# Optimization experiments

Measured on AMD Instinct MI355X. Metric: run time of the kernel, lower is better.

Reference implementation:

```python
import jax, jax.numpy as jnp
import numpy as np

N = 50000   # nodes
E = 800000  # edges
F = 64      # node_feature_dim
H = 128     # hidden_dim


def setup_inputs() -> dict:
    key = jax.random.key(0)
    ks = jax.random.split(key, 20)
    def w(k, shape, fan_in):
        return jax.random.normal(k, shape, jnp.float32) / np.sqrt(fan_in)
    return {
        "x": jax.random.normal(ks[0], (N, F), jnp.float32),
        "edge_index": jax.random.randint(ks[1], (2, E), 0, N, jnp.int32),
        "enc_w1": w(ks[2], (F, H), F), "enc_b1": jnp.zeros((H,), jnp.float32),
        "enc_w2": w(ks[3], (H, H), H), "enc_b2": jnp.zeros((H,), jnp.float32),
        "w_c1": w(ks[4], (H, H), H), "b_c1": jnp.zeros((H,), jnp.float32),
        "w_c2": w(ks[5], (H, H), H), "b_c2": jnp.zeros((H,), jnp.float32),
        "w_c3": w(ks[6], (H, H), H), "b_c3": jnp.zeros((H,), jnp.float32),
        "dec_w1": w(ks[7], (H, H), H), "dec_b1": jnp.zeros((H,), jnp.float32),
        "dec_w2": w(ks[8], (H, F), H), "dec_b2": jnp.zeros((F,), jnp.float32),
    }


def _gcn_conv(h, W, b, src, dst, dinv):
    # PyG GCNConv: D^-1/2 (A+I) D^-1/2 (h W) + b  (self-loops already in src/dst)
    hw = h @ W                                   # [N, H]
    norm = dinv[src] * dinv[dst]                 # [E+N]
    msg = hw[src] * norm[:, None]                # gather + scale
    return jax.ops.segment_sum(msg, dst, num_segments=N) + b


def reference(x, edge_index, enc_w1, enc_b1, enc_w2, enc_b2,
              w_c1, b_c1, w_c2, b_c2, w_c3, b_c3,
              dec_w1, dec_b1, dec_w2, dec_b2):
    loop = jnp.arange(N, dtype=edge_index.dtype)
    src = jnp.concatenate([edge_index[0], loop])
    dst = jnp.concatenate([edge_index[1], loop])
    deg = jax.ops.segment_sum(jnp.ones_like(dst, jnp.float32), dst, num_segments=N)
    dinv = jax.lax.rsqrt(deg)  # deg >= 1 because of self-loops

    h = jax.nn.relu(x @ enc_w1 + enc_b1) @ enc_w2 + enc_b2  # encoder MLP
    h = jax.nn.relu(_gcn_conv(h, w_c1, b_c1, src, dst, dinv))
    h = jax.nn.relu(_gcn_conv(h, w_c2, b_c2, src, dst, dinv))
    h = jax.nn.relu(_gcn_conv(h, w_c3, b_c3, src, dst, dinv))
    # window_size == 1: chunk+cat is identity
    out = jax.nn.relu(h @ dec_w1 + dec_b1) @ dec_w2 + dec_b2  # decoder MLP
    return jax.nn.sigmoid(out)
```

## Files before the change

### kernel.cpp

```cpp
#include <hip/hip_runtime.h>
#include <stdint.h>

#define NN 50000
#define NE 800000
#define FD 64
#define HD 128
#define NBKT 196
#define BCAP 5120
#define P1E 8192

static_assert(NN % 16 == 0, "aggm16 grid is exact");

typedef __attribute__((ext_vector_type(8))) short short8;
typedef __attribute__((ext_vector_type(4))) float f32x4;

#define AS1 __attribute__((address_space(1)))
#define AS3 __attribute__((address_space(3)))

__device__ __forceinline__ float bflo(unsigned int v) {
    union { unsigned int u; float f; } c; c.u = v << 16; return c.f;
}
__device__ __forceinline__ float bfhi(unsigned int v) {
    union { unsigned int u; float f; } c; c.u = v & 0xffff0000u; return c.f;
}
__device__ __forceinline__ unsigned short f2bf(float f) {
    union { float f; unsigned int u; } c; c.f = f;
    unsigned int u = c.u;
    return (unsigned short)((u + 0x7fffu + ((u >> 16) & 1u)) >> 16);
}
__device__ __forceinline__ unsigned int pack2(float a, float b) {
    return (unsigned int)f2bf(a) | ((unsigned int)f2bf(b) << 16);
}

__global__ void wt0_k(const float* __restrict__ w0, unsigned short* __restrict__ t0) {
    int e = blockIdx.x * 256 + threadIdx.x;
    int k = e >> 7, c = e & 127;
    int gsw = (k >> 3) ^ (c & 7);
    t0[c * 64 + gsw * 8 + (k & 7)] = f2bf(w0[e]);
}

template <int K, int COLS, int EPI, bool BIAS, bool RSCALE, bool A_F32, bool OUT_F32>
__device__ __forceinline__ void mgemm_dev(
    int bid,
    const void* __restrict__ Av,
    const unsigned short* __restrict__ Wt,
    const float* __restrict__ bias,
    const float* __restrict__ dinv,
    void* __restrict__ outv, int nrows)
{
    constexpr int NB = COLS / 16;
    constexpr int KC = K / 32;
    constexpr int GMASK = (K >> 3) - 1;
    __shared__ __align__(16) unsigned char Ws8[COLS * K * 2];

    const int tid = threadIdx.x;
    const int wave = tid >> 6;
    const int lane = tid & 63;

    {
        constexpr int ROUNDS = COLS * K * 2 / 4096;
        const int gb = wave * 1024 + lane * 16;
        const int lb = wave * 1024;
        #pragma unroll
        for (int r = 0; r < ROUNDS; r++) {
            __builtin_amdgcn_global_load_lds(
                (const AS1 unsigned int*)((const unsigned char*)Wt + r * 4096 + gb),
                (AS3 unsigned int*)(Ws8 + r * 4096 + lb),
                16, 0, 0);
        }
    }

    const int m = lane & 15;
    const int q = lane >> 4;
    const int row0 = bid * 64 + wave * 16;

    f32x4 acc[NB];
    #pragma unroll
    for (int i = 0; i < NB; i++) acc[i] = (f32x4){0.f, 0.f, 0.f, 0.f};

    const bool arow_ok = !A_F32 || (row0 + m) < nrows;

    short8 af[KC];
    #pragma unroll
    for (int kc = 0; kc < KC; kc++) {
        if constexpr (A_F32) {
            const float* arowf = (const float*)Av + (size_t)(row0 + m) * K + q * 8 + kc * 32;
            float4 lo = make_float4(0.f, 0.f, 0.f, 0.f), hi = lo;
            if (arow_ok) { lo = *(const float4*)arowf; hi = *(const float4*)(arowf + 4); }
            af[kc][0] = (short)f2bf(lo.x); af[kc][1] = (short)f2bf(lo.y);
            af[kc][2] = (short)f2bf(lo.z); af[kc][3] = (short)f2bf(lo.w);
            af[kc][4] = (short)f2bf(hi.x); af[kc][5] = (short)f2bf(hi.y);
            af[kc][6] = (short)f2bf(hi.z); af[kc][7] = (short)f2bf(hi.w);
        } else {
            const unsigned short* arow = (const unsigned short*)Av + (size_t)(row0 + m) * K + q * 8 + kc * 32;
            af[kc] = *(const short8*)arow;
        }
    }
    __syncthreads();

    #pragma unroll
    for (int kc = 0; kc < KC; kc++) {
        #pragma unroll
        for (int nb = 0; nb < NB; nb++) {
            const int c = nb * 16 + m;
            const int gsw = (kc * 4 + q) ^ (c & GMASK);
            short8 bf = *(const short8*)&Ws8[(c * K + gsw * 8) * 2];
            acc[nb] = __builtin_amdgcn_mfma_f32_16x16x32_bf16(af[kc], bf, acc[nb], 0, 0, 0);
        }
    }

    float bv[NB];
    #pragma unroll
    for (int nb = 0; nb < NB; nb++) bv[nb] = BIAS ? bias[nb * 16 + m] : 0.f;

    #pragma unroll
    for (int r = 0; r < 4; r++) {
        int row = row0 + q * 4 + r;
        if (row < nrows) {
            float sc = RSCALE ? dinv[row] : 1.f;
            #pragma unroll
            for (int nb = 0; nb < NB; nb++) {
                float t = acc[nb][r];
                if (RSCALE) t *= sc;
                t += bv[nb];
                if (EPI == 1) t = fmaxf(t, 0.f);
                if (EPI == 2) t = 1.f / (1.f + __expf(-t));
                if constexpr (OUT_F32) {
                    ((float*)outv)[(size_t)row * COLS + nb * 16 + m] = t;
                } else {
                    ((unsigned short*)outv)[(size_t)row * COLS + nb * 16 + m] = f2bf(t);
                }
            }
        }
    }
}

template <int K, int COLS, int EPI, bool BIAS, bool RSCALE, bool A_F32, bool OUT_F32>
__global__ __launch_bounds__(256) void mgemm_k(
    const void* __restrict__ Av, const unsigned short* __restrict__ Wt,
    const float* __restrict__ bias, const float* __restrict__ dinv,
    void* __restrict__ outv, int nrows)
{
    mgemm_dev<K, COLS, EPI, BIAS, RSCALE, A_F32, OUT_F32>(blockIdx.x, Av, Wt, bias, dinv, outv, nrows);
}

__global__ __launch_bounds__(256) void k1_k(
    const float* __restrict__ x, const unsigned short* __restrict__ t0s,
    const float* __restrict__ enc_b1, unsigned short* __restrict__ bufA,
    const int* __restrict__ src, const int* __restrict__ dst,
    int* __restrict__ gcnt, unsigned int* __restrict__ bucket,
    const float* __restrict__ w1, const float* __restrict__ w2,
    const float* __restrict__ w3, const float* __restrict__ w4,
    const float* __restrict__ w5, const float* __restrict__ w6,
    unsigned short* __restrict__ t1, unsigned short* __restrict__ t2,
    unsigned short* __restrict__ t3, unsigned short* __restrict__ t4,
    unsigned short* __restrict__ t5, unsigned short* __restrict__ t6,
    int gb, int pb)
{
    const int b = blockIdx.x;
    if (b < gb) {
        mgemm_dev<64, 128, 1, true, false, true, false>(b, x, t0s, enc_b1, nullptr, bufA, NN);
    } else if (b < gb + pb) {
        __shared__ int lcnt[256], lsw[256], lexc[256], lofs[256], lrank[256];
        __shared__ unsigned int stage[P1E];
        const int tid = threadIdx.x;
        const int bb = b - gb;
        lcnt[tid] = 0; lrank[tid] = 0;
        __syncthreads();
        unsigned int ent[P1E / 256];
        #pragma unroll
        for (int u = 0; u < P1E / 256; u++) {
            int g = bb * P1E + u * 256 + tid;
            if (g < NE) {
                int d = dst[g], s = src[g];
                int bk = d >> 8;
                atomicAdd(&lcnt[bk], 1);
                ent[u] = (unsigned int)s | ((unsigned int)(d & 255) << 16)
                       | ((unsigned int)bk << 24);
            } else ent[u] = 0xFFFFFFFFu;
        }
        __syncthreads();
        int v = lcnt[tid];
        lsw[tid] = v; __syncthreads();
        for (int d = 1; d < 256; d <<= 1) {
            int xx = (tid >= d) ? lsw[tid - d] : 0; __syncthreads();
            lsw[tid] += xx; __syncthreads();
        }
        lexc[tid] = lsw[tid] - v;
        lofs[tid] = (v > 0) ? atomicAdd(&gcnt[tid], v) : 0;
        __syncthreads();
        #pragma unroll
        for (int u = 0; u < P1E / 256; u++) {
            if (ent[u] != 0xFFFFFFFFu) {
                int bk = ent[u] >> 24;
                int r = atomicAdd(&lrank[bk], 1);
                stage[lexc[bk] + r] = ent[u];
            }
        }
        __syncthreads();
        int cb = NE - bb * P1E; if (cb > P1E) cb = P1E;
        for (int i = tid; i < cb; i += 256) {
            unsigned int e = stage[i];
            int bk = e >> 24;
            bucket[(size_t)bk * BCAP + lofs[bk] + (i - lexc[bk])] = e;
        }
    } else {
        int b2 = b - gb - pb;
        const float* W; unsigned short* T; int C = 128;
        if      (b2 <  64) { W = w1; T = t1; }
        else if (b2 < 128) { W = w2; T = t2; b2 -= 64; }
        else if (b2 < 192) { W = w3; T = t3; b2 -= 128; }
        else if (b2 < 256) { W = w4; T = t4; b2 -= 192; }
        else if (b2 < 320) { W = w5; T = t5; b2 -= 256; }
        else               { W = w6; T = t6; b2 -= 320; C = 64; }
        int e = b2 * 256 + threadIdx.x;
        int k, c;
        if (C == 128) { k = e >> 7; c = e & 127; } else { k = e >> 6; c = e & 63; }
        int gsw = (k >> 3) ^ (c & 15);
        T[c * 128 + gsw * 8 + (k & 7)] = f2bf(W[e]);
    }
}

__global__ __launch_bounds__(256) void k2_k(
    const unsigned short* __restrict__ bufA, const unsigned short* __restrict__ t1,
    const float* __restrict__ enc_b2, unsigned short* __restrict__ bufB,
    const int* __restrict__ gcnt, const unsigned int* __restrict__ bucket,
    int* __restrict__ off, float* __restrict__ dinv,
    unsigned short* __restrict__ csr, int gb)
{
    if ((int)blockIdx.x < gb) {
        mgemm_dev<128, 128, 0, true, false, false, false>(blockIdx.x, bufA, t1, enc_b2, nullptr, bufB, NN);
    } else {
        __shared__ int lc[256], sw[256], sexc[256], lr[256], gsh[256];
        const int tid = threadIdx.x;
        const int b = blockIdx.x - gb;
        int gv = (tid < NBKT) ? gcnt[tid] : 0;
        gsh[tid] = gv; __syncthreads();
        for (int d = 1; d < 256; d <<= 1) {
            int xx = (tid >= d) ? gsh[tid - d] : 0; __syncthreads();
            gsh[tid] += xx; __syncthreads();
        }
        const int cb = gcnt[b];
        const int base = gsh[b] - cb;
        unsigned int ent[BCAP / 256];
        #pragma unroll
        for (int u = 0; u < BCAP / 256; u++) {
            int i = u * 256 + tid;
            ent[u] = (i < cb) ? bucket[(size_t)b * BCAP + i] : 0xFFFFFFFFu;
        }
        lc[tid] = 0; lr[tid] = 0;
        __syncthreads();
        #pragma unroll
        for (int u = 0; u < BCAP / 256; u++)
            if (ent[u] != 0xFFFFFFFFu) atomicAdd(&lc[(ent[u] >> 16) & 255], 1);
        __syncthreads();
        int v = lc[tid];
        int node = b * 256 + tid;
        if (node < NN) dinv[node] = rsqrtf((float)(v + 1));
        sw[tid] = v; __syncthreads();
        for (int d = 1; d < 256; d <<= 1) {
            int xx = (tid >= d) ? sw[tid - d] : 0; __syncthreads();
            sw[tid] += xx; __syncthreads();
        }
        sexc[tid] = sw[tid] - v;
        if (node < NN) off[node] = base + sexc[tid];
        if (b == NBKT - 1 && tid == 0) off[NN] = NE;
        __syncthreads();
        #pragma unroll
        for (int u = 0; u < BCAP / 256; u++) {
            if (ent[u] != 0xFFFFFFFFu) {
                int dl = (ent[u] >> 16) & 255;
                int r = atomicAdd(&lr[dl], 1);
                csr[base + sexc[dl] + r] = (unsigned short)(ent[u] & 0xffff);
            }
        }
    }
}

__device__ __forceinline__ void gather16_dev(
    const uint4* __restrict__ hws, const int* __restrict__ off,
    const unsigned short* __restrict__ csr, const float* __restrict__ dinv,
    const float* __restrict__ gbias, uint4* __restrict__ g4, int bid, int tid)
{
    const int g = tid >> 4;
    const int l = tid & 15;
    const int row = bid * 16 + g;
    const float4 b0 = *(const float4*)(gbias + 8 * l);
    const float4 b1 = *(const float4*)(gbias + 8 * l + 4);

    uint4 v = hws[(size_t)row * 16 + l];
    float s0 = bflo(v.x), s1 = bfhi(v.x), s2 = bflo(v.y), s3 = bfhi(v.y);
    float s4 = bflo(v.z), s5 = bfhi(v.z), s6 = bflo(v.w), s7 = bfhi(v.w);
    const int je = off[row + 1];
    int j = off[row];
    for (; j + 8 <= je; j += 8) {
        uint4 t[8];
        #pragma unroll
        for (int u = 0; u < 8; u++) t[u] = hws[(size_t)csr[j + u] * 16 + l];
        #pragma unroll
        for (int u = 0; u < 8; u++) {
            s0 += bflo(t[u].x); s1 += bfhi(t[u].x);
            s2 += bflo(t[u].y); s3 += bfhi(t[u].y);
            s4 += bflo(t[u].z); s5 += bfhi(t[u].z);
            s6 += bflo(t[u].w); s7 += bfhi(t[u].w);
        }
    }
    for (; j < je; j++) {
        uint4 t = hws[(size_t)csr[j] * 16 + l];
        s0 += bflo(t.x); s1 += bfhi(t.x);
        s2 += bflo(t.y); s3 += bfhi(t.y);
        s4 += bflo(t.z); s5 += bfhi(t.z);
        s6 += bflo(t.w); s7 += bfhi(t.w);
    }
    const float di = dinv[row];
    uint4 o;
    o.x = pack2(fmaxf(fmaf(di, s0, b0.x), 0.f), fmaxf(fmaf(di, s1, b0.y), 0.f));
    o.y = pack2(fmaxf(fmaf(di, s2, b0.z), 0.f), fmaxf(fmaf(di, s3, b0.w), 0.f));
    o.z = pack2(fmaxf(fmaf(di, s4, b1.x), 0.f), fmaxf(fmaf(di, s5, b1.y), 0.f));
    o.w = pack2(fmaxf(fmaf(di, s6, b1.z), 0.f), fmaxf(fmaf(di, s7, b1.w), 0.f));
    g4[g * 16 + (l ^ g)] = o;
}

template <int EPI, bool BIAS, bool RSCALE>
__global__ __launch_bounds__(256) void aggm16_k(
    const uint4* __restrict__ hws, const int* __restrict__ off,
    const unsigned short* __restrict__ csr, const float* __restrict__ dinv,
    const float* __restrict__ gbias,
    const unsigned short* __restrict__ Wt,
    const float* __restrict__ obias,
    unsigned short* __restrict__ out)
{
    __shared__ __align__(16) uint4 g4[16 * 16];

    const int tid = threadIdx.x;
    const int bid = blockIdx.x;
    const int wave = tid >> 6;
    const int lane = tid & 63;
    const int m = lane & 15;
    const int q = lane >> 4;

    short8 Bf0[4], Bf1[4];
    #pragma unroll
    for (int kc = 0; kc < 4; kc++) {
        const int c0 = wave * 32 + m;
        const int c1 = c0 + 16;
        Bf0[kc] = *(const short8*)&Wt[c0 * 128 + (((kc * 4 + q) ^ (c0 & 15)) << 3)];
        Bf1[kc] = *(const short8*)&Wt[c1 * 128 + (((kc * 4 + q) ^ (c1 & 15)) << 3)];
    }

    gather16_dev(hws, off, csr, dinv, gbias, g4, bid, tid);
    __syncthreads();

    f32x4 a0 = (f32x4){0.f, 0.f, 0.f, 0.f}, a1 = a0;
    #pragma unroll
    for (int kc = 0; kc < 4; kc++) {
        short8 af = *(const short8*)&g4[m * 16 + ((q + kc * 4) ^ m)];
        a0 = __builtin_amdgcn_mfma_f32_16x16x32_bf16(af, Bf0[kc], a0, 0, 0, 0);
        a1 = __builtin_amdgcn_mfma_f32_16x16x32_bf16(af, Bf1[kc], a1, 0, 0, 0);
    }

    const int c0 = wave * 32 + m;
    const int c1 = c0 + 16;
    const float bv0 = BIAS ? obias[c0] : 0.f;
    const float bv1 = BIAS ? obias[c1] : 0.f;

    #pragma unroll
    for (int r = 0; r < 4; r++) {
        const int row = bid * 16 + q * 4 + r;
        const float sc = RSCALE ? dinv[row] : 1.f;
        float t0 = a0[r], t1 = a1[r];
        if (RSCALE) { t0 *= sc; t1 *= sc; }
        t0 += bv0; t1 += bv1;
        if (EPI == 1) { t0 = fmaxf(t0, 0.f); t1 = fmaxf(t1, 0.f); }
        out[(size_t)row * 128 + c0] = f2bf(t0);
        out[(size_t)row * 128 + c1] = f2bf(t1);
    }
}

__global__ __launch_bounds__(256) void decf16_k(
    const uint4* __restrict__ hws, const int* __restrict__ off,
    const unsigned short* __restrict__ csr, const float* __restrict__ dinv,
    const float* __restrict__ gbias,
    const unsigned short* __restrict__ Wt1,
    const float* __restrict__ db1,
    const unsigned short* __restrict__ Wt2,
    const float* __restrict__ db2,
    float* __restrict__ outp)
{
    __shared__ __align__(16) uint4 g4[16 * 16];
    __shared__ __align__(16) uint4 h4[16 * 16];

    const int tid = threadIdx.x;
    const int bid = blockIdx.x;
    const int wave = tid >> 6;
    const int lane = tid & 63;
    const int m = lane & 15;
    const int q = lane >> 4;

    short8 Wf0[4], Wf1[4];
    #pragma unroll
    for (int kc = 0; kc < 4; kc++) {
        const int c0 = wave * 32 + m;
        const int c1 = c0 + 16;
        Wf0[kc] = *(const short8*)&Wt1[c0 * 128 + (((kc * 4 + q) ^ (c0 & 15)) << 3)];
        Wf1[kc] = *(const short8*)&Wt1[c1 * 128 + (((kc * 4 + q) ^ (c1 & 15)) << 3)];
    }

    gather16_dev(hws, off, csr, dinv, gbias, g4, bid, tid);
    __syncthreads();

    f32x4 at0 = (f32x4){0.f, 0.f, 0.f, 0.f}, at1 = at0;
    #pragma unroll
    for (int kc = 0; kc < 4; kc++) {
        short8 gf = *(const short8*)&g4[m * 16 + ((q + kc * 4) ^ m)];
        at0 = __builtin_amdgcn_mfma_f32_16x16x32_bf16(Wf0[kc], gf, at0, 0, 0, 0);
        at1 = __builtin_amdgcn_mfma_f32_16x16x32_bf16(Wf1[kc], gf, at1, 0, 0, 0);
    }

    short8 Bf2[4];
    #pragma unroll
    for (int kc = 0; kc < 4; kc++) {
        const int c = wave * 16 + m;
        Bf2[kc] = *(const short8*)&Wt2[c * 128 + (((kc * 4 + q) ^ (c & 15)) << 3)];
    }

    {
        uint2* h2 = (uint2*)h4;
        {
            const int F = wave * 32 + q * 4;
            const float4 bb = *(const float4*)(db1 + F);
            float v0 = fmaxf(at0[0] + bb.x, 0.f);
            float v1 = fmaxf(at0[1] + bb.y, 0.f);
            float v2 = fmaxf(at0[2] + bb.z, 0.f);
            float v3 = fmaxf(at0[3] + bb.w, 0.f);
            uint2 hv; hv.x = pack2(v0, v1); hv.y = pack2(v2, v3);
            const int cf = wave * 4 + (q >> 1);
            h2[m * 32 + (((cf ^ m) << 1) | (q & 1))] = hv;
        }
        {
            const int F = wave * 32 + 16 + q * 4;
            const float4 bb = *(const float4*)(db1 + F);
            float v0 = fmaxf(at1[0] + bb.x, 0.f);
            float v1 = fmaxf(at1[1] + bb.y, 0.f);
            float v2 = fmaxf(at1[2] + bb.z, 0.f);
            float v3 = fmaxf(at1[3] + bb.w, 0.f);
            uint2 hv; hv.x = pack2(v0, v1); hv.y = pack2(v2, v3);
            const int cf = wave * 4 + 2 + (q >> 1);
            h2[m * 32 + (((cf ^ m) << 1) | (q & 1))] = hv;
        }
    }
    __syncthreads();

    f32x4 a2 = (f32x4){0.f, 0.f, 0.f, 0.f};
    #pragma unroll
    for (int kc = 0; kc < 4; kc++) {
        short8 af = *(const short8*)&h4[m * 16 + ((q + kc * 4) ^ m)];
        a2 = __builtin_amdgcn_mfma_f32_16x16x32_bf16(af, Bf2[kc], a2, 0, 0, 0);
    }

    const int c = wave * 16 + m;
    const float bv = db2[c];
    #pragma unroll
    for (int r = 0; r < 4; r++) {
        const int row = bid * 16 + q * 4 + r;
        float t = a2[r] + bv;
        t = 1.f / (1.f + __expf(-t));
        outp[(size_t)row * 64 + c] = t;
    }
}

extern "C" void kernel_launch(void* const* d_in, const int* in_sizes, int n_in,
                              void* d_out, int out_size, void* d_ws, size_t ws_size,
                              hipStream_t stream)
{
    const float* x      = (const float*)d_in[0];
    const int*   ei     = (const int*)d_in[1];
    const float* enc_w1 = (const float*)d_in[2];
    const float* enc_b1 = (const float*)d_in[3];
    const float* enc_w2 = (const float*)d_in[4];
    const float* enc_b2 = (const float*)d_in[5];
    const float* w_c1   = (const float*)d_in[6];
    const float* b_c1   = (const float*)d_in[7];
    const float* w_c2   = (const float*)d_in[8];
    const float* b_c2   = (const float*)d_in[9];
    const float* w_c3   = (const float*)d_in[10];
    const float* b_c3   = (const float*)d_in[11];
    const float* dec_w1 = (const float*)d_in[12];
    const float* dec_b1 = (const float*)d_in[13];
    const float* dec_w2 = (const float*)d_in[14];
    const float* dec_b2 = (const float*)d_in[15];

    const int* src = ei;
    const int* dst = ei + NE;

    const int NP = 50048;

    char* ws = (char*)d_ws;
    size_t o = 0;
    auto alloc = [&](size_t bytes) -> void* {
        void* p = ws + o;
        o = (o + bytes + 255) & ~(size_t)255;
        return p;
    };
    int*   gcnt = (int*)alloc(256 * 4);
    int*   off  = (int*)alloc((size_t)(NN + 1) * 4);
    unsigned short* csr = (unsigned short*)alloc((size_t)NE * 2);
    unsigned int* bucket = (unsigned int*)alloc((size_t)NBKT * BCAP * 4);
    float* dinv = (float*)alloc((size_t)NN * 4);
    unsigned short* bufA = (unsigned short*)alloc((size_t)NP * HD * 2);
    unsigned short* bufB = (unsigned short*)alloc((size_t)NP * HD * 2);
    unsigned short* t0 = (unsigned short*)alloc(64 * 128 * 2);
    unsigned short* t1 = (unsigned short*)alloc(128 * 128 * 2);
    unsigned short* t2 = (unsigned short*)alloc(128 * 128 * 2);
    unsigned short* t3 = (unsigned short*)alloc(128 * 128 * 2);
    unsigned short* t4 = (unsigned short*)alloc(128 * 128 * 2);
    unsigned short* t5 = (unsigned short*)alloc(128 * 128 * 2);
    unsigned short* t6 = (unsigned short*)alloc(128 * 64 * 2);
    (void)ws_size; (void)n_in; (void)in_sizes; (void)out_size;

    hipMemsetAsync(gcnt, 0, 256 * 4, stream);

    const int PB   = (NE + P1E - 1) / P1E;
    const int GB   = NP / 64;
    const int GB16 = NN / 16;

    wt0_k<<<32, 256, 0, stream>>>(enc_w1, t0);
    k1_k<<<GB + PB + 352, 256, 0, stream>>>(x, t0, enc_b1, bufA, src, dst, gcnt, bucket,
                                            enc_w2, w_c1, w_c2, w_c3, dec_w1, dec_w2,
                                            t1, t2, t3, t4, t5, t6, GB, PB);
    k2_k<<<GB + NBKT, 256, 0, stream>>>(bufA, t1, enc_b2, bufB, gcnt, bucket,
                                        off, dinv, csr, GB);
    mgemm_k<128, 128, 0, false, true, false, false><<<GB, 256, 0, stream>>>(bufB, t2, nullptr, dinv, bufA, NN);
    aggm16_k<0, false, true><<<GB16, 256, 0, stream>>>((const uint4*)bufA, off, csr, dinv, b_c1, t3, nullptr, bufB);
    aggm16_k<0, false, true><<<GB16, 256, 0, stream>>>((const uint4*)bufB, off, csr, dinv, b_c2, t4, nullptr, bufA);
    decf16_k<<<GB16, 256, 0, stream>>>((const uint4*)bufA, off, csr, dinv, b_c3,
                                       t5, dec_b1, t6, dec_b2, (float*)d_out);
}
```

Before: 272.2 us.

## Fuse encoder second layer with first conv GEMM and balance edge gather per block

The second encoder GEMM and the first GCN weight multiply now run in one kernel that keeps the intermediate 16-row tile in LDS, which removes a separate GEMM launch and a full bufA round trip. The first conv's dinv[src] scaling moves from the GEMM epilogue into a weighted gather. The per-row gather is replaced by an edge-balanced scheme: each 16-thread group takes an equal slice of the block's edges and flushes partial sums into a shared fp32 accumulator with LDS atomics. This evens out work across rows with different degrees, at the cost of LDS atomics, extra syncs and more shared memory per block.

```diff
diff --git a/kernel.cpp b/kernel.cpp
--- a/kernel.cpp
+++ b/kernel.cpp
@@ -9,7 +9,7 @@
 #define BCAP 5120
 #define P1E 8192
 
-static_assert(NN % 16 == 0, "aggm16 grid is exact");
+static_assert(NN % 16 == 0, "16-row tiles are exact");
 
 typedef __attribute__((ext_vector_type(8))) short short8;
 typedef __attribute__((ext_vector_type(4))) float f32x4;
@@ -39,13 +39,12 @@
     t0[c * 64 + gsw * 8 + (k & 7)] = f2bf(w0[e]);
 }
 
-template <int K, int COLS, int EPI, bool BIAS, bool RSCALE, bool A_F32, bool OUT_F32>
+template <int K, int COLS, int EPI, bool BIAS, bool A_F32>
 __device__ __forceinline__ void mgemm_dev(
     int bid,
     const void* __restrict__ Av,
     const unsigned short* __restrict__ Wt,
     const float* __restrict__ bias,
-    const float* __restrict__ dinv,
     void* __restrict__ outv, int nrows)
 {
     constexpr int NB = COLS / 16;
@@ -117,31 +116,14 @@
     for (int r = 0; r < 4; r++) {
         int row = row0 + q * 4 + r;
         if (row < nrows) {
-            float sc = RSCALE ? dinv[row] : 1.f;
             #pragma unroll
             for (int nb = 0; nb < NB; nb++) {
-                float t = acc[nb][r];
-                if (RSCALE) t *= sc;
-                t += bv[nb];
+                float t = acc[nb][r] + bv[nb];
                 if (EPI == 1) t = fmaxf(t, 0.f);
-                if (EPI == 2) t = 1.f / (1.f + __expf(-t));
-                if constexpr (OUT_F32) {
-                    ((float*)outv)[(size_t)row * COLS + nb * 16 + m] = t;
-                } else {
-                    ((unsigned short*)outv)[(size_t)row * COLS + nb * 16 + m] = f2bf(t);
-                }
+                ((unsigned short*)outv)[(size_t)row * COLS + nb * 16 + m] = f2bf(t);
             }
         }
     }
-}
-
-template <int K, int COLS, int EPI, bool BIAS, bool RSCALE, bool A_F32, bool OUT_F32>
-__global__ __launch_bounds__(256) void mgemm_k(
-    const void* __restrict__ Av, const unsigned short* __restrict__ Wt,
-    const float* __restrict__ bias, const float* __restrict__ dinv,
-    void* __restrict__ outv, int nrows)
-{
-    mgemm_dev<K, COLS, EPI, BIAS, RSCALE, A_F32, OUT_F32>(blockIdx.x, Av, Wt, bias, dinv, outv, nrows);
 }
 
 __global__ __launch_bounds__(256) void k1_k(
@@ -159,7 +141,7 @@
 {
     const int b = blockIdx.x;
     if (b < gb) {
-        mgemm_dev<64, 128, 1, true, false, true, false>(b, x, t0s, enc_b1, nullptr, bufA, NN);
+        mgemm_dev<64, 128, 1, true, true>(b, x, t0s, enc_b1, bufA, NN);
     } else if (b < gb + pb) {
         __shared__ int lcnt[256], lsw[256], lexc[256], lofs[256], lrank[256];
         __shared__ unsigned int stage[P1E];
@@ -221,15 +203,86 @@
     }
 }
 
-__global__ __launch_bounds__(256) void k2_k(
+__global__ __launch_bounds__(256) void k2f_k(
     const unsigned short* __restrict__ bufA, const unsigned short* __restrict__ t1,
-    const float* __restrict__ enc_b2, unsigned short* __restrict__ bufB,
+    const float* __restrict__ enc_b2, const unsigned short* __restrict__ t2,
+    unsigned short* __restrict__ bufB,
     const int* __restrict__ gcnt, const unsigned int* __restrict__ bucket,
     int* __restrict__ off, float* __restrict__ dinv,
     unsigned short* __restrict__ csr, int gb)
 {
     if ((int)blockIdx.x < gb) {
-        mgemm_dev<128, 128, 0, true, false, false, false>(blockIdx.x, bufA, t1, enc_b2, nullptr, bufB, NN);
+        __shared__ __align__(16) uint4 h4[16 * 16];
+        const int tid = threadIdx.x;
+        const int wave = tid >> 6;
+        const int lane = tid & 63;
+        const int m = lane & 15;
+        const int q = lane >> 4;
+        const int row0 = blockIdx.x * 16;
+
+        short8 Wf0[4], Wf1[4];
+        #pragma unroll
+        for (int kc = 0; kc < 4; kc++) {
+            const int c0 = wave * 32 + m;
+            const int c1 = c0 + 16;
+            Wf0[kc] = *(const short8*)&t1[c0 * 128 + (((kc * 4 + q) ^ (c0 & 15)) << 3)];
+            Wf1[kc] = *(const short8*)&t1[c1 * 128 + (((kc * 4 + q) ^ (c1 & 15)) << 3)];
+        }
+
+        f32x4 at0 = (f32x4){0.f, 0.f, 0.f, 0.f}, at1 = at0;
+        #pragma unroll
+        for (int kc = 0; kc < 4; kc++) {
+            short8 gf = *(const short8*)&bufA[(size_t)(row0 + m) * 128 + ((q + kc * 4) << 3)];
+            at0 = __builtin_amdgcn_mfma_f32_16x16x32_bf16(Wf0[kc], gf, at0, 0, 0, 0);
+            at1 = __builtin_amdgcn_mfma_f32_16x16x32_bf16(Wf1[kc], gf, at1, 0, 0, 0);
+        }
+
+        {
+            uint2* h2 = (uint2*)h4;
+            {
+                const int F = wave * 32 + q * 4;
+                const float4 bb = *(const float4*)(enc_b2 + F);
+                uint2 hv;
+                hv.x = pack2(at0[0] + bb.x, at0[1] + bb.y);
+                hv.y = pack2(at0[2] + bb.z, at0[3] + bb.w);
+                const int cf = wave * 4 + (q >> 1);
+                h2[m * 32 + (((cf ^ m) << 1) | (q & 1))] = hv;
+            }
+            {
+                const int F = wave * 32 + 16 + q * 4;
+                const float4 bb = *(const float4*)(enc_b2 + F);
+                uint2 hv;
+                hv.x = pack2(at1[0] + bb.x, at1[1] + bb.y);
+                hv.y = pack2(at1[2] + bb.z, at1[3] + bb.w);
+                const int cf = wave * 4 + 2 + (q >> 1);
+                h2[m * 32 + (((cf ^ m) << 1) | (q & 1))] = hv;
+            }
+        }
+        __syncthreads();
+
+        short8 Bf0[4], Bf1[4];
+        #pragma unroll
+        for (int kc = 0; kc < 4; kc++) {
+            const int c0 = wave * 32 + m;
+            const int c1 = c0 + 16;
+            Bf0[kc] = *(const short8*)&t2[c0 * 128 + (((kc * 4 + q) ^ (c0 & 15)) << 3)];
+            Bf1[kc] = *(const short8*)&t2[c1 * 128 + (((kc * 4 + q) ^ (c1 & 15)) << 3)];
+        }
+        f32x4 a0 = (f32x4){0.f, 0.f, 0.f, 0.f}, a1 = a0;
+        #pragma unroll
+        for (int kc = 0; kc < 4; kc++) {
+            short8 af = *(const short8*)&h4[m * 16 + ((q + kc * 4) ^ m)];
+            a0 = __builtin_amdgcn_mfma_f32_16x16x32_bf16(af, Bf0[kc], a0, 0, 0, 0);
+            a1 = __builtin_amdgcn_mfma_f32_16x16x32_bf16(af, Bf1[kc], a1, 0, 0, 0);
+        }
+        const int c0 = wave * 32 + m;
+        const int c1 = c0 + 16;
+        #pragma unroll
+        for (int r = 0; r < 4; r++) {
+            const int row = row0 + q * 4 + r;
+            bufB[(size_t)row * 128 + c0] = f2bf(a0[r]);
+            bufB[(size_t)row * 128 + c1] = f2bf(a1[r]);
+        }
     } else {
         __shared__ int lc[256], sw[256], sexc[256], lr[256], gsh[256];
         const int tid = threadIdx.x;
@@ -277,63 +330,115 @@
     }
 }
 
-__device__ __forceinline__ void gather16_dev(
+template <bool WEIGHTED>
+__device__ __forceinline__ void gatherb_dev(
     const uint4* __restrict__ hws, const int* __restrict__ off,
     const unsigned short* __restrict__ csr, const float* __restrict__ dinv,
-    const float* __restrict__ gbias, uint4* __restrict__ g4, int bid, int tid)
+    float* __restrict__ accf, int* __restrict__ offw, int bid, int tid)
 {
     const int g = tid >> 4;
     const int l = tid & 15;
-    const int row = bid * 16 + g;
-    const float4 b0 = *(const float4*)(gbias + 8 * l);
-    const float4 b1 = *(const float4*)(gbias + 8 * l + 4);
-
-    uint4 v = hws[(size_t)row * 16 + l];
-    float s0 = bflo(v.x), s1 = bfhi(v.x), s2 = bflo(v.y), s3 = bfhi(v.y);
-    float s4 = bflo(v.z), s5 = bfhi(v.z), s6 = bflo(v.w), s7 = bfhi(v.w);
-    const int je = off[row + 1];
-    int j = off[row];
-    for (; j + 8 <= je; j += 8) {
-        uint4 t[8];
-        #pragma unroll
-        for (int u = 0; u < 8; u++) t[u] = hws[(size_t)csr[j + u] * 16 + l];
+    if (tid < 17) offw[tid] = off[bid * 16 + tid];
+    {
+        const int row = bid * 16 + g;
+        uint4 v = hws[(size_t)row * 16 + l];
+        const float w = WEIGHTED ? dinv[row] : 1.f;
+        float* a = accf + g * 128 + l * 8;
+        a[0] = w * bflo(v.x); a[1] = w * bfhi(v.x);
+        a[2] = w * bflo(v.y); a[3] = w * bfhi(v.y);
+        a[4] = w * bflo(v.z); a[5] = w * bfhi(v.z);
+        a[6] = w * bflo(v.w); a[7] = w * bfhi(v.w);
+    }
+    __syncthreads();
+
+    const int e0 = offw[0];
+    const int len = offw[16] - e0;
+    const int js = e0 + ((len * g) >> 4);
+    const int je = e0 + ((len * (g + 1)) >> 4);
+
+    int d = 0;
+    #pragma unroll
+    for (int i = 1; i < 16; i++) d = (offw[i] <= js) ? i : d;
+    int nb = offw[d + 1];
+
+    float s[8];
+    #pragma unroll
+    for (int i = 0; i < 8; i++) s[i] = 0.f;
+
+    for (int j = js; j < je; j += 8) {
+        uint4 t[8]; float dw[8];
         #pragma unroll
         for (int u = 0; u < 8; u++) {
-            s0 += bflo(t[u].x); s1 += bfhi(t[u].x);
-            s2 += bflo(t[u].y); s3 += bfhi(t[u].y);
-            s4 += bflo(t[u].z); s5 += bfhi(t[u].z);
-            s6 += bflo(t[u].w); s7 += bfhi(t[u].w);
-        }
-    }
-    for (; j < je; j++) {
-        uint4 t = hws[(size_t)csr[j] * 16 + l];
-        s0 += bflo(t.x); s1 += bfhi(t.x);
-        s2 += bflo(t.y); s3 += bfhi(t.y);
-        s4 += bflo(t.z); s5 += bfhi(t.z);
-        s6 += bflo(t.w); s7 += bfhi(t.w);
-    }
+            int jj = j + u; jj = (jj < je) ? jj : (je - 1);
+            const int idx = (int)csr[jj];
+            t[u] = hws[(size_t)idx * 16 + l];
+            dw[u] = WEIGHTED ? dinv[idx] : 1.f;
+        }
+        #pragma unroll
+        for (int u = 0; u < 8; u++) {
+            const int jj = j + u;
+            if (jj < je) {
+                while (jj >= nb) {
+                    float* a = accf + d * 128 + l * 8;
+                    #pragma unroll
+                    for (int i = 0; i < 8; i++) { atomicAdd(a + i, s[i]); s[i] = 0.f; }
+                    d++; nb = offw[d + 1];
+                }
+                const float w = dw[u];
+                s[0] = fmaf(w, bflo(t[u].x), s[0]); s[1] = fmaf(w, bfhi(t[u].x), s[1]);
+                s[2] = fmaf(w, bflo(t[u].y), s[2]); s[3] = fmaf(w, bfhi(t[u].y), s[3]);
+                s[4] = fmaf(w, bflo(t[u].z), s[4]); s[5] = fmaf(w, bfhi(t[u].z), s[5]);
+                s[6] = fmaf(w, bflo(t[u].w), s[6]); s[7] = fmaf(w, bfhi(t[u].w), s[7]);
+            }
+        }
+    }
+    if (js < je) {
+        float* a = accf + d * 128 + l * 8;
+        #pragma unroll
+        for (int i = 0; i < 8; i++) atomicAdd(a + i, s[i]);
+    }
+}
+
+__device__ __forceinline__ void gepi_dev(
+    const float* __restrict__ accf, const float* __restrict__ dinv,
+    const float* __restrict__ gbias, uint4* __restrict__ g4, int bid, int tid)
+{
+    const int r = tid >> 4;
+    const int c = tid & 15;
+    const int row = bid * 16 + r;
     const float di = dinv[row];
+    const float* a = accf + r * 128 + c * 8;
+    float4 v0 = *(const float4*)a;
+    float4 v1 = *(const float4*)(a + 4);
+    const float4 b0 = *(const float4*)(gbias + c * 8);
+    const float4 b1 = *(const float4*)(gbias + c * 8 + 4);
     uint4 o;
-    o.x = pack2(fmaxf(fmaf(di, s0, b0.x), 0.f), fmaxf(fmaf(di, s1, b0.y), 0.f));
-    o.y = pack2(fmaxf(fmaf(di, s2, b0.z), 0.f), fmaxf(fmaf(di, s3, b0.w), 0.f));
-    o.z = pack2(fmaxf(fmaf(di, s4, b1.x), 0.f), fmaxf(fmaf(di, s5, b1.y), 0.f));
-    o.w = pack2(fmaxf(fmaf(di, s6, b1.z), 0.f), fmaxf(fmaf(di, s7, b1.w), 0.f));
-    g4[g * 16 + (l ^ g)] = o;
-}
-
-template <int EPI, bool BIAS, bool RSCALE>
+    o.x = pack2(fmaxf(fmaf(di, v0.x, b0.x), 0.f), fmaxf(fmaf(di, v0.y, b0.y), 0.f));
+    o.y = pack2(fmaxf(fmaf(di, v0.z, b0.z), 0.f), fmaxf(fmaf(di, v0.w, b0.w), 0.f));
+    o.z = pack2(fmaxf(fmaf(di, v1.x, b1.x), 0.f), fmaxf(fmaf(di, v1.y, b1.y), 0.f));
+    o.w = pack2(fmaxf(fmaf(di, v1.z, b1.z), 0.f), fmaxf(fmaf(di, v1.w, b1.w), 0.f));
+    g4[r * 16 + (c ^ r)] = o;
+}
+
+template <bool WEIGHTED>
 __global__ __launch_bounds__(256) void aggm16_k(
     const uint4* __restrict__ hws, const int* __restrict__ off,
     const unsigned short* __restrict__ csr, const float* __restrict__ dinv,
-    const float* __restrict__ gbias,
-    const unsigned short* __restrict__ Wt,
-    const float* __restrict__ obias,
+    const float* __restrict__ gbias, const unsigned short* __restrict__ Wt,
     unsigned short* __restrict__ out)
 {
-    __shared__ __align__(16) uint4 g4[16 * 16];
+    __shared__ float accf[16 * 128];
+    __shared__ int offw[17];
+    __shared__ __align__(16) uint4 g4t[16 * 16];
 
     const int tid = threadIdx.x;
     const int bid = blockIdx.x;
+
+    gatherb_dev<WEIGHTED>(hws, off, csr, dinv, accf, offw, bid, tid);
+    __syncthreads();
+    gepi_dev(accf, dinv, gbias, g4t, bid, tid);
+    __syncthreads();
+
     const int wave = tid >> 6;
     const int lane = tid & 63;
     const int m = lane & 15;
@@ -347,33 +452,21 @@
         Bf0[kc] = *(const short8*)&Wt[c0 * 128 + (((kc * 4 + q) ^ (c0 & 15)) << 3)];
         Bf1[kc] = *(const short8*)&Wt[c1 * 128 + (((kc * 4 + q) ^ (c1 & 15)) << 3)];
     }
-
-    gather16_dev(hws, off, csr, dinv, gbias, g4, bid, tid);
-    __syncthreads();
-
     f32x4 a0 = (f32x4){0.f, 0.f, 0.f, 0.f}, a1 = a0;
     #pragma unroll
     for (int kc = 0; kc < 4; kc++) {
-        short8 af = *(const short8*)&g4[m * 16 + ((q + kc * 4) ^ m)];
+        short8 af = *(const short8*)&g4t[m * 16 + ((q + kc * 4) ^ m)];
         a0 = __builtin_amdgcn_mfma_f32_16x16x32_bf16(af, Bf0[kc], a0, 0, 0, 0);
         a1 = __builtin_amdgcn_mfma_f32_16x16x32_bf16(af, Bf1[kc], a1, 0, 0, 0);
     }
-
     const int c0 = wave * 32 + m;
     const int c1 = c0 + 16;
-    const float bv0 = BIAS ? obias[c0] : 0.f;
-    const float bv1 = BIAS ? obias[c1] : 0.f;
-
     #pragma unroll
     for (int r = 0; r < 4; r++) {
         const int row = bid * 16 + q * 4 + r;
-        const float sc = RSCALE ? dinv[row] : 1.f;
-        float t0 = a0[r], t1 = a1[r];
-        if (RSCALE) { t0 *= sc; t1 *= sc; }
-        t0 += bv0; t1 += bv1;
-        if (EPI == 1) { t0 = fmaxf(t0, 0.f); t1 = fmaxf(t1, 0.f); }
-        out[(size_t)row * 128 + c0] = f2bf(t0);
-        out[(size_t)row * 128 + c1] = f2bf(t1);
+        const float sc = dinv[row];
+        out[(size_t)row * 128 + c0] = f2bf(a0[r] * sc);
+        out[(size_t)row * 128 + c1] = f2bf(a1[r] * sc);
     }
 }
 
@@ -387,11 +480,19 @@
     const float* __restrict__ db2,
     float* __restrict__ outp)
 {
-    __shared__ __align__(16) uint4 g4[16 * 16];
+    __shared__ float accf[16 * 128];
+    __shared__ int offw[17];
+    __shared__ __align__(16) uint4 g4t[16 * 16];
     __shared__ __align__(16) uint4 h4[16 * 16];
 
     const int tid = threadIdx.x;
     const int bid = blockIdx.x;
+
+    gatherb_dev<false>(hws, off, csr, dinv, accf, offw, bid, tid);
+    __syncthreads();
+    gepi_dev(accf, dinv, gbias, g4t, bid, tid);
+    __syncthreads();
+
     const int wave = tid >> 6;
     const int lane = tid & 63;
     const int m = lane & 15;
@@ -405,14 +506,10 @@
         Wf0[kc] = *(const short8*)&Wt1[c0 * 128 + (((kc * 4 + q) ^ (c0 & 15)) << 3)];
         Wf1[kc] = *(const short8*)&Wt1[c1 * 128 + (((kc * 4 + q) ^ (c1 & 15)) << 3)];
     }
-
-    gather16_dev(hws, off, csr, dinv, gbias, g4, bid, tid);
-    __syncthreads();
-
     f32x4 at0 = (f32x4){0.f, 0.f, 0.f, 0.f}, at1 = at0;
     #pragma unroll
     for (int kc = 0; kc < 4; kc++) {
-        short8 gf = *(const short8*)&g4[m * 16 + ((q + kc * 4) ^ m)];
+        short8 gf = *(const short8*)&g4t[m * 16 + ((q + kc * 4) ^ m)];
         at0 = __builtin_amdgcn_mfma_f32_16x16x32_bf16(Wf0[kc], gf, at0, 0, 0, 0);
         at1 = __builtin_amdgcn_mfma_f32_16x16x32_bf16(Wf1[kc], gf, at1, 0, 0, 0);
     }
@@ -429,22 +526,18 @@
         {
             const int F = wave * 32 + q * 4;
             const float4 bb = *(const float4*)(db1 + F);
-            float v0 = fmaxf(at0[0] + bb.x, 0.f);
-            float v1 = fmaxf(at0[1] + bb.y, 0.f);
-            float v2 = fmaxf(at0[2] + bb.z, 0.f);
-            float v3 = fmaxf(at0[3] + bb.w, 0.f);
-            uint2 hv; hv.x = pack2(v0, v1); hv.y = pack2(v2, v3);
+            uint2 hv;
+            hv.x = pack2(fmaxf(at0[0] + bb.x, 0.f), fmaxf(at0[1] + bb.y, 0.f));
+            hv.y = pack2(fmaxf(at0[2] + bb.z, 0.f), fmaxf(at0[3] + bb.w, 0.f));
             const int cf = wave * 4 + (q >> 1);
             h2[m * 32 + (((cf ^ m) << 1) | (q & 1))] = hv;
         }
         {
             const int F = wave * 32 + 16 + q * 4;
             const float4 bb = *(const float4*)(db1 + F);
-            float v0 = fmaxf(at1[0] + bb.x, 0.f);
-            float v1 = fmaxf(at1[1] + bb.y, 0.f);
-            float v2 = fmaxf(at1[2] + bb.z, 0.f);
-            float v3 = fmaxf(at1[3] + bb.w, 0.f);
-            uint2 hv; hv.x = pack2(v0, v1); hv.y = pack2(v2, v3);
+            uint2 hv;
+            hv.x = pack2(fmaxf(at1[0] + bb.x, 0.f), fmaxf(at1[1] + bb.y, 0.f));
+            hv.y = pack2(fmaxf(at1[2] + bb.z, 0.f), fmaxf(at1[3] + bb.w, 0.f));
             const int cf = wave * 4 + 2 + (q >> 1);
             h2[m * 32 + (((cf ^ m) << 1) | (q & 1))] = hv;
         }
@@ -457,7 +550,6 @@
         short8 af = *(const short8*)&h4[m * 16 + ((q + kc * 4) ^ m)];
         a2 = __builtin_amdgcn_mfma_f32_16x16x32_bf16(af, Bf2[kc], a2, 0, 0, 0);
     }
-
     const int c = wave * 16 + m;
     const float bv = db2[c];
     #pragma unroll
@@ -528,11 +620,10 @@
     k1_k<<<GB + PB + 352, 256, 0, stream>>>(x, t0, enc_b1, bufA, src, dst, gcnt, bucket,
                                             enc_w2, w_c1, w_c2, w_c3, dec_w1, dec_w2,
                                             t1, t2, t3, t4, t5, t6, GB, PB);
-    k2_k<<<GB + NBKT, 256, 0, stream>>>(bufA, t1, enc_b2, bufB, gcnt, bucket,
-                                        off, dinv, csr, GB);
-    mgemm_k<128, 128, 0, false, true, false, false><<<GB, 256, 0, stream>>>(bufB, t2, nullptr, dinv, bufA, NN);
-    aggm16_k<0, false, true><<<GB16, 256, 0, stream>>>((const uint4*)bufA, off, csr, dinv, b_c1, t3, nullptr, bufB);
-    aggm16_k<0, false, true><<<GB16, 256, 0, stream>>>((const uint4*)bufB, off, csr, dinv, b_c2, t4, nullptr, bufA);
-    decf16_k<<<GB16, 256, 0, stream>>>((const uint4*)bufA, off, csr, dinv, b_c3,
+    k2f_k<<<GB16 + NBKT, 256, 0, stream>>>(bufA, t1, enc_b2, t2, bufB,
+                                           gcnt, bucket, off, dinv, csr, GB16);
+    aggm16_k<true><<<GB16, 256, 0, stream>>>((const uint4*)bufB, off, csr, dinv, b_c1, t3, bufA);
+    aggm16_k<false><<<GB16, 256, 0, stream>>>((const uint4*)bufA, off, csr, dinv, b_c2, t4, bufB);
+    decf16_k<<<GB16, 256, 0, stream>>>((const uint4*)bufB, off, csr, dinv, b_c3,
                                        t5, dec_b1, t6, dec_b2, (float*)d_out);
 }
```

Result: slower. 365.9 us (+34.4%).

## Fold first weight conversion into encoder GEMM, sort gather rows by degree

Applied to the files above, without the earlier changes.

The separate kernel that converted enc_w1 to swizzled bf16 is removed; each encoder GEMM block now converts the fp32 weight straight into shared memory, which saves one launch but repeats the conversion in every block. The 16-row gather now stages the row offsets in shared memory and ranks rows by degree, so groups of lanes that sit next to each other in a wave handle rows of similar length and divergence drops, at the cost of an extra sync and a small sort. The edge-partition chunk size is also halved, which doubles the number of partition blocks.

```diff
diff --git a/kernel.cpp b/kernel.cpp
--- a/kernel.cpp
+++ b/kernel.cpp
@@ -7,9 +7,9 @@
 #define HD 128
 #define NBKT 196
 #define BCAP 5120
-#define P1E 8192
-
-static_assert(NN % 16 == 0, "aggm16 grid is exact");
+#define P1E 4096
+
+static_assert(NN % 16 == 0, "16-row tiles are exact");
 
 typedef __attribute__((ext_vector_type(8))) short short8;
 typedef __attribute__((ext_vector_type(4))) float f32x4;
@@ -32,18 +32,11 @@
     return (unsigned int)f2bf(a) | ((unsigned int)f2bf(b) << 16);
 }
 
-__global__ void wt0_k(const float* __restrict__ w0, unsigned short* __restrict__ t0) {
-    int e = blockIdx.x * 256 + threadIdx.x;
-    int k = e >> 7, c = e & 127;
-    int gsw = (k >> 3) ^ (c & 7);
-    t0[c * 64 + gsw * 8 + (k & 7)] = f2bf(w0[e]);
-}
-
-template <int K, int COLS, int EPI, bool BIAS, bool RSCALE, bool A_F32, bool OUT_F32>
+template <int K, int COLS, int EPI, bool BIAS, bool RSCALE, bool A_F32, bool OUT_F32, bool WCVT>
 __device__ __forceinline__ void mgemm_dev(
     int bid,
     const void* __restrict__ Av,
-    const unsigned short* __restrict__ Wt,
+    const void* __restrict__ Wt,
     const float* __restrict__ bias,
     const float* __restrict__ dinv,
     void* __restrict__ outv, int nrows)
@@ -57,7 +50,17 @@
     const int wave = tid >> 6;
     const int lane = tid & 63;
 
-    {
+    if constexpr (WCVT) {
+        const float* wf = (const float*)Wt;
+        unsigned short* ws = (unsigned short*)Ws8;
+        #pragma unroll
+        for (int i = 0; i < K * COLS / 256; i++) {
+            const int e = i * 256 + tid;
+            const int k = e / COLS, c = e % COLS;
+            const int gsw = (k >> 3) ^ (c & GMASK);
+            ws[c * K + gsw * 8 + (k & 7)] = f2bf(wf[e]);
+        }
+    } else {
         constexpr int ROUNDS = COLS * K * 2 / 4096;
         const int gb = wave * 1024 + lane * 16;
         const int lb = wave * 1024;
@@ -141,11 +144,11 @@
     const float* __restrict__ bias, const float* __restrict__ dinv,
     void* __restrict__ outv, int nrows)
 {
-    mgemm_dev<K, COLS, EPI, BIAS, RSCALE, A_F32, OUT_F32>(blockIdx.x, Av, Wt, bias, dinv, outv, nrows);
+    mgemm_dev<K, COLS, EPI, BIAS, RSCALE, A_F32, OUT_F32, false>(blockIdx.x, Av, Wt, bias, dinv, outv, nrows);
 }
 
 __global__ __launch_bounds__(256) void k1_k(
-    const float* __restrict__ x, const unsigned short* __restrict__ t0s,
+    const float* __restrict__ x, const float* __restrict__ w0,
     const float* __restrict__ enc_b1, unsigned short* __restrict__ bufA,
     const int* __restrict__ src, const int* __restrict__ dst,
     int* __restrict__ gcnt, unsigned int* __restrict__ bucket,
@@ -159,7 +162,7 @@
 {
     const int b = blockIdx.x;
     if (b < gb) {
-        mgemm_dev<64, 128, 1, true, false, true, false>(b, x, t0s, enc_b1, nullptr, bufA, NN);
+        mgemm_dev<64, 128, 1, true, false, true, false, true>(b, x, w0, enc_b1, nullptr, bufA, NN);
     } else if (b < gb + pb) {
         __shared__ int lcnt[256], lsw[256], lexc[256], lofs[256], lrank[256];
         __shared__ unsigned int stage[P1E];
@@ -229,7 +232,7 @@
     unsigned short* __restrict__ csr, int gb)
 {
     if ((int)blockIdx.x < gb) {
-        mgemm_dev<128, 128, 0, true, false, false, false>(blockIdx.x, bufA, t1, enc_b2, nullptr, bufB, NN);
+        mgemm_dev<128, 128, 0, true, false, false, false, false>(blockIdx.x, bufA, t1, enc_b2, nullptr, bufB, NN);
     } else {
         __shared__ int lc[256], sw[256], sexc[256], lr[256], gsh[256];
         const int tid = threadIdx.x;
@@ -280,19 +283,38 @@
 __device__ __forceinline__ void gather16_dev(
     const uint4* __restrict__ hws, const int* __restrict__ off,
     const unsigned short* __restrict__ csr, const float* __restrict__ dinv,
-    const float* __restrict__ gbias, uint4* __restrict__ g4, int bid, int tid)
-{
+    const float* __restrict__ gbias, uint4* __restrict__ g4,
+    int* __restrict__ ish, int bid, int tid)
+{
+    int* offw = ish;
+    int* perm = ish + 17;
     const int g = tid >> 4;
     const int l = tid & 15;
-    const int row = bid * 16 + g;
+
+    if (tid < 17) offw[tid] = off[bid * 16 + tid];
+    __syncthreads();
+    if (tid < 16) {
+        const int dg = offw[tid + 1] - offw[tid];
+        int r = 0;
+        #pragma unroll
+        for (int j = 0; j < 16; j++) {
+            const int dj = offw[j + 1] - offw[j];
+            r += (dj > dg) || (dj == dg && j < tid);
+        }
+        perm[r] = tid;
+    }
+    __syncthreads();
+
+    const int rr = perm[g];
+    const int row = bid * 16 + rr;
     const float4 b0 = *(const float4*)(gbias + 8 * l);
     const float4 b1 = *(const float4*)(gbias + 8 * l + 4);
 
     uint4 v = hws[(size_t)row * 16 + l];
     float s0 = bflo(v.x), s1 = bfhi(v.x), s2 = bflo(v.y), s3 = bfhi(v.y);
     float s4 = bflo(v.z), s5 = bfhi(v.z), s6 = bflo(v.w), s7 = bfhi(v.w);
-    const int je = off[row + 1];
-    int j = off[row];
+    const int je = offw[rr + 1];
+    int j = offw[rr];
     for (; j + 8 <= je; j += 8) {
         uint4 t[8];
         #pragma unroll
@@ -318,7 +340,7 @@
     o.y = pack2(fmaxf(fmaf(di, s2, b0.z), 0.f), fmaxf(fmaf(di, s3, b0.w), 0.f));
     o.z = pack2(fmaxf(fmaf(di, s4, b1.x), 0.f), fmaxf(fmaf(di, s5, b1.y), 0.f));
     o.w = pack2(fmaxf(fmaf(di, s6, b1.z), 0.f), fmaxf(fmaf(di, s7, b1.w), 0.f));
-    g4[g * 16 + (l ^ g)] = o;
+    g4[rr * 16 + (l ^ rr)] = o;
 }
 
 template <int EPI, bool BIAS, bool RSCALE>
@@ -331,6 +353,7 @@
     unsigned short* __restrict__ out)
 {
     __shared__ __align__(16) uint4 g4[16 * 16];
+    __shared__ int ish[33];
 
     const int tid = threadIdx.x;
     const int bid = blockIdx.x;
@@ -348,7 +371,7 @@
         Bf1[kc] = *(const short8*)&Wt[c1 * 128 + (((kc * 4 + q) ^ (c1 & 15)) << 3)];
     }
 
-    gather16_dev(hws, off, csr, dinv, gbias, g4, bid, tid);
+    gather16_dev(hws, off, csr, dinv, gbias, g4, ish, bid, tid);
     __syncthreads();
 
     f32x4 a0 = (f32x4){0.f, 0.f, 0.f, 0.f}, a1 = a0;
@@ -389,6 +412,7 @@
 {
     __shared__ __align__(16) uint4 g4[16 * 16];
     __shared__ __align__(16) uint4 h4[16 * 16];
+    __shared__ int ish[33];
 
     const int tid = threadIdx.x;
     const int bid = blockIdx.x;
@@ -406,7 +430,7 @@
         Wf1[kc] = *(const short8*)&Wt1[c1 * 128 + (((kc * 4 + q) ^ (c1 & 15)) << 3)];
     }
 
-    gather16_dev(hws, off, csr, dinv, gbias, g4, bid, tid);
+    gather16_dev(hws, off, csr, dinv, gbias, g4, ish, bid, tid);
     __syncthreads();
 
     f32x4 at0 = (f32x4){0.f, 0.f, 0.f, 0.f}, at1 = at0;
@@ -429,22 +453,18 @@
         {
             const int F = wave * 32 + q * 4;
             const float4 bb = *(const float4*)(db1 + F);
-            float v0 = fmaxf(at0[0] + bb.x, 0.f);
-            float v1 = fmaxf(at0[1] + bb.y, 0.f);
-            float v2 = fmaxf(at0[2] + bb.z, 0.f);
-            float v3 = fmaxf(at0[3] + bb.w, 0.f);
-            uint2 hv; hv.x = pack2(v0, v1); hv.y = pack2(v2, v3);
+            uint2 hv;
+            hv.x = pack2(fmaxf(at0[0] + bb.x, 0.f), fmaxf(at0[1] + bb.y, 0.f));
+            hv.y = pack2(fmaxf(at0[2] + bb.z, 0.f), fmaxf(at0[3] + bb.w, 0.f));
             const int cf = wave * 4 + (q >> 1);
             h2[m * 32 + (((cf ^ m) << 1) | (q & 1))] = hv;
         }
         {
             const int F = wave * 32 + 16 + q * 4;
             const float4 bb = *(const float4*)(db1 + F);
-            float v0 = fmaxf(at1[0] + bb.x, 0.f);
-            float v1 = fmaxf(at1[1] + bb.y, 0.f);
-            float v2 = fmaxf(at1[2] + bb.z, 0.f);
-            float v3 = fmaxf(at1[3] + bb.w, 0.f);
-            uint2 hv; hv.x = pack2(v0, v1); hv.y = pack2(v2, v3);
+            uint2 hv;
+            hv.x = pack2(fmaxf(at1[0] + bb.x, 0.f), fmaxf(at1[1] + bb.y, 0.f));
+            hv.y = pack2(fmaxf(at1[2] + bb.z, 0.f), fmaxf(at1[3] + bb.w, 0.f));
             const int cf = wave * 4 + 2 + (q >> 1);
             h2[m * 32 + (((cf ^ m) << 1) | (q & 1))] = hv;
         }
@@ -509,7 +529,6 @@
     float* dinv = (float*)alloc((size_t)NN * 4);
     unsigned short* bufA = (unsigned short*)alloc((size_t)NP * HD * 2);
     unsigned short* bufB = (unsigned short*)alloc((size_t)NP * HD * 2);
-    unsigned short* t0 = (unsigned short*)alloc(64 * 128 * 2);
     unsigned short* t1 = (unsigned short*)alloc(128 * 128 * 2);
     unsigned short* t2 = (unsigned short*)alloc(128 * 128 * 2);
     unsigned short* t3 = (unsigned short*)alloc(128 * 128 * 2);
@@ -524,8 +543,7 @@
     const int GB   = NP / 64;
     const int GB16 = NN / 16;
 
-    wt0_k<<<32, 256, 0, stream>>>(enc_w1, t0);
-    k1_k<<<GB + PB + 352, 256, 0, stream>>>(x, t0, enc_b1, bufA, src, dst, gcnt, bucket,
+    k1_k<<<GB + PB + 352, 256, 0, stream>>>(x, enc_w1, enc_b1, bufA, src, dst, gcnt, bucket,
                                             enc_w2, w_c1, w_c2, w_c3, dec_w1, dec_w2,
                                             t1, t2, t3, t4, t5, t6, GB, PB);
     k2_k<<<GB + NBKT, 256, 0, stream>>>(bufA, t1, enc_b2, bufB, gcnt, bucket,
```

New measurement: 278.4 us. 1.02x slower.
